# Kernel tuning notes

Hardware: AMD Instinct MI355X
Metric: run time of the kernel (lower is better)

The kernel has to match this reference:

```python
import jax, jax.numpy as jnp
import numpy as np

HEADS = 16
NEG = -1.0e9


def setup_inputs() -> dict:
    key = jax.random.key(0)
    ks = jax.random.split(key, 9)
    B, T, E = 2, 2048, 1024
    s = 1.0 / np.sqrt(E)
    return {
        "x": jax.random.normal(ks[0], (B, T, E), dtype=jnp.float32),
        "Wq": jax.random.normal(ks[1], (E, E), dtype=jnp.float32) * s,
        "bq": jax.random.normal(ks[2], (E,), dtype=jnp.float32) * 0.01,
        "Wk": jax.random.normal(ks[3], (E, E), dtype=jnp.float32) * s,
        "bk": jax.random.normal(ks[4], (E,), dtype=jnp.float32) * 0.01,
        "Wv": jax.random.normal(ks[5], (E, E), dtype=jnp.float32) * s,
        "bv": jax.random.normal(ks[6], (E,), dtype=jnp.float32) * 0.01,
        "Wo": jax.random.normal(ks[7], (E, E), dtype=jnp.float32) * s,
        "bo": jax.random.normal(ks[8], (E,), dtype=jnp.float32) * 0.01,
    }


def reference(x, Wq, bq, Wk, bk, Wv, bv, Wo, bo):
    B, T, E = x.shape
    H = HEADS
    D = E // H
    # In the original forward (idx_t=-2, context=None): context = x, so
    # values(x), keys(context), queries(context) all read x.
    v = (x @ Wv + bv).reshape(B, T, H, D)
    k = (x @ Wk + bk).reshape(B, T, H, D)
    q = (x @ Wq + bq).reshape(B, T, H, D)
    # causal mask: 1 above diagonal, 0 on/below; broadcast over (B, H)
    mask = 1.0 - jnp.tril(jnp.ones((T, T), dtype=x.dtype))  # [T, T]
    energy = jnp.einsum("bqhd,bkhd->bhqk", q, k)
    # Faithful to source: mask*(-1e9) added BEFORE the sqrt(embed_size) scaling
    energy = energy + mask[None, None] * jnp.asarray(NEG, dtype=x.dtype)
    attn = jax.nn.softmax(energy / jnp.sqrt(jnp.asarray(E, dtype=x.dtype)), axis=-1)
    out = jnp.einsum("bhqk,bkhd->bqhd", attn, v).reshape(B, T, E)
    return out @ Wo + bo
```

## Files before the change

### kernel.cpp

```cpp
#include <hip/hip_runtime.h>
#include <hip/hip_bf16.h>
#include <stdint.h>


typedef __attribute__((ext_vector_type(8))) short short8;
typedef __attribute__((ext_vector_type(4))) short short4v;
typedef __attribute__((ext_vector_type(4))) float f32x4;

#define MFMA16(a, b, c) __builtin_amdgcn_mfma_f32_16x16x32_bf16((a), (b), (c), 0, 0, 0)

static __device__ __forceinline__ unsigned short f2bf(float f) {
    union { float f; unsigned int u; } v; v.f = f;
    unsigned int r = v.u + 0x7fffu + ((v.u >> 16) & 1u);
    return (unsigned short)(r >> 16);
}
static __device__ __forceinline__ void gload16(const unsigned short* g,
                                               unsigned short* l) {
    __builtin_amdgcn_global_load_lds(
        (const __attribute__((address_space(1))) void*)g,
        (__attribute__((address_space(3))) void*)l, 16, 0, 0);
}

__global__ __launch_bounds__(256) void k_convert_x(const float* __restrict__ x,
                                                   unsigned short* __restrict__ xb) {
    int i = blockIdx.x * 256 + threadIdx.x;
    const float4* p = (const float4*)(x + (size_t)i * 8);
    float4 a = p[0], b = p[1];
    short8 o;
    o[0] = (short)f2bf(a.x); o[1] = (short)f2bf(a.y);
    o[2] = (short)f2bf(a.z); o[3] = (short)f2bf(a.w);
    o[4] = (short)f2bf(b.x); o[5] = (short)f2bf(b.y);
    o[6] = (short)f2bf(b.z); o[7] = (short)f2bf(b.w);
    ((short8*)xb)[i] = o;
}

__global__ __launch_bounds__(256) void k_transpose_w4(
        const float* __restrict__ W0, const float* __restrict__ W1,
        const float* __restrict__ W2, const float* __restrict__ W3,
        unsigned short* __restrict__ T0, unsigned short* __restrict__ T1,
        unsigned short* __restrict__ T2, unsigned short* __restrict__ T3) {
    const float* W = (blockIdx.z == 0) ? W0 : (blockIdx.z == 1) ? W1
                     : (blockIdx.z == 2) ? W2 : W3;
    unsigned short* Wt = (blockIdx.z == 0) ? T0 : (blockIdx.z == 1) ? T1
                         : (blockIdx.z == 2) ? T2 : T3;
    __shared__ float tw[64][68];
    const int k0 = blockIdx.x * 64, n0 = blockIdx.y * 64;
    const int tid = threadIdx.x;
#pragma unroll
    for (int r = 0; r < 4; ++r) {
        int i = tid + r * 256;
        int row = i >> 4, c4 = (i & 15) * 4;
        float4 v = *(const float4*)(W + (size_t)(k0 + row) * 1024 + n0 + c4);
        *(float4*)(&tw[row][c4]) = v;
    }
    __syncthreads();
#pragma unroll
    for (int r = 0; r < 2; ++r) {
        int i = tid + r * 256;
        int nrow = i >> 3, kc = (i & 7) * 8;
        short8 o;
#pragma unroll
        for (int j = 0; j < 8; ++j) o[j] = (short)f2bf(tw[kc + j][nrow]);
        *(short8*)(Wt + (size_t)(n0 + nrow) * 1024 + k0 + kc) = o;
    }
}

template <int MODE>
__global__ __launch_bounds__(256) void k_gemm2(const unsigned short* __restrict__ A,
                                               const unsigned short* __restrict__ Bt,
                                               const float* __restrict__ bq,
                                               const float* __restrict__ bk,
                                               const float* __restrict__ bv,
                                               unsigned short* __restrict__ Qb,
                                               unsigned short* __restrict__ Kb,
                                               unsigned short* __restrict__ Vt,
                                               float* __restrict__ Co) {
    __shared__ unsigned short As[128 * 32];
    __shared__ unsigned short Bs[128 * 32];
    const int tid = threadIdx.x;
    const int w = tid >> 6, lane = tid & 63;
    const int quad = lane >> 4, l16 = lane & 15;
    const int wm = w >> 1, wn = w & 1;
    const int m0 = blockIdx.x * 128, n0 = blockIdx.y * 128;
    const int lrow = lane >> 2, lch = (lane & 3) * 8;

    const unsigned short* ga = A + (size_t)(m0 + w * 32 + lrow) * 1024 + lch;
    const unsigned short* gb = Bt + (size_t)(n0 + w * 32 + lrow) * 1024 + lch;
    unsigned short* la0 = &As[(w * 32) * 32];
    unsigned short* la1 = &As[(w * 32 + 16) * 32];
    unsigned short* lb0 = &Bs[(w * 32) * 32];
    unsigned short* lb1 = &Bs[(w * 32 + 16) * 32];

    f32x4 acc[4][4];
#pragma unroll
    for (int mt = 0; mt < 4; ++mt)
#pragma unroll
        for (int nt = 0; nt < 4; ++nt) acc[mt][nt] = (f32x4){0.f, 0.f, 0.f, 0.f};

    for (int k0 = 0; k0 < 1024; k0 += 32) {
        __syncthreads();
        gload16(ga + k0, la0);
        gload16(ga + 16 * 1024 + k0, la1);
        gload16(gb + k0, lb0);
        gload16(gb + 16 * 1024 + k0, lb1);
        __syncthreads();
        short8 af[4], bf[4];
#pragma unroll
        for (int mt = 0; mt < 4; ++mt)
            af[mt] = *(const short8*)(&As[(wm * 64 + mt * 16 + l16) * 32 + quad * 8]);
#pragma unroll
        for (int nt = 0; nt < 4; ++nt)
            bf[nt] = *(const short8*)(&Bs[(wn * 64 + nt * 16 + l16) * 32 + quad * 8]);
#pragma unroll
        for (int mt = 0; mt < 4; ++mt)
#pragma unroll
            for (int nt = 0; nt < 4; ++nt)
                acc[mt][nt] = MFMA16(af[mt], bf[nt], acc[mt][nt]);
    }

    if (MODE == 1) {
#pragma unroll
        for (int nt = 0; nt < 4; ++nt) {
            int col = n0 + wn * 64 + nt * 16 + l16;
            float bb = bq[col];
#pragma unroll
            for (int mt = 0; mt < 4; ++mt) {
                int row = m0 + wm * 64 + mt * 16 + quad * 4;
#pragma unroll
                for (int r = 0; r < 4; ++r)
                    Co[(size_t)(row + r) * 1024 + col] = acc[mt][nt][r] + bb;
            }
        }
    } else if (n0 < 2048) {
        unsigned short* C = (n0 < 1024) ? Qb : Kb;
        const float* bias = (n0 < 1024) ? bq : bk;
        int cb = (n0 < 1024) ? n0 : (n0 - 1024);
#pragma unroll
        for (int nt = 0; nt < 4; ++nt) {
            int col = cb + wn * 64 + nt * 16 + l16;
            float bb = bias[col];
#pragma unroll
            for (int mt = 0; mt < 4; ++mt) {
                int row = m0 + wm * 64 + mt * 16 + quad * 4;
#pragma unroll
                for (int r = 0; r < 4; ++r)
                    C[(size_t)(row + r) * 1024 + col] = f2bf(acc[mt][nt][r] + bb);
            }
        }
    } else {
#pragma unroll
        for (int nt = 0; nt < 4; ++nt) {
            int vcol = (n0 - 2048) + wn * 64 + nt * 16 + l16;
            float bb = bv[vcol];
#pragma unroll
            for (int mt = 0; mt < 4; ++mt) {
                int row = m0 + wm * 64 + mt * 16 + quad * 4;
                int b = row >> 11, t = row & 2047;
                short4v o;
#pragma unroll
                for (int r = 0; r < 4; ++r) o[r] = (short)f2bf(acc[mt][nt][r] + bb);
                *(short4v*)(&Vt[((size_t)(b * 16 + (vcol >> 6)) * 64 + (vcol & 63))
                                    * 2048 + t]) = o;
            }
        }
    }
}

__global__ __launch_bounds__(256) void k_attn(const unsigned short* __restrict__ Qb,
                                              const unsigned short* __restrict__ Kb,
                                              const unsigned short* __restrict__ Vt,
                                              unsigned short* __restrict__ Ob) {
    __shared__ unsigned short Ks[2][64][72];
    __shared__ unsigned short Vs[2][64][72];
    __shared__ unsigned short Ps[4][16][72];
    const int tid = threadIdx.x;
    const int w = tid >> 6, lane = tid & 63;
    const int quad = lane >> 4, l16 = lane & 15;
    const int id = blockIdx.x;
    const int bh = (id & 7) + 8 * ((id >> 3) & 3);
    const int qb = 31 - (id >> 5);
    const int b = bh >> 4, h = bh & 15;
    const float scale = 0.03125f;
    const int qg = qb * 64 + w * 16 + l16;
    const f32x4 zero4 = {0.f, 0.f, 0.f, 0.f};

    const int srow = tid >> 3, sc8 = (tid & 7) * 8;
    const unsigned short* kg0 = Kb + (size_t)(b * 2048) * 1024 + h * 64 + sc8;
    const unsigned short* vg0 = Vt + (size_t)(bh * 64 + srow) * 2048 + sc8;

    short8 qf[2];
    {
        const unsigned short* qp =
            Qb + (size_t)(b * 2048 + qg) * 1024 + h * 64 + quad * 8;
        qf[0] = *(const short8*)(qp);
        qf[1] = *(const short8*)(qp + 32);
    }
    float m_ = -1e30f, l_ = 0.f;
    f32x4 o[4];
#pragma unroll
    for (int dt = 0; dt < 4; ++dt) o[dt] = zero4;

    short8 kr0, kr1, vr0, vr1;
    kr0 = *(const short8*)(kg0 + (size_t)(srow) * 1024);
    kr1 = *(const short8*)(kg0 + (size_t)(32 + srow) * 1024);
    vr0 = *(const short8*)(vg0);
    vr1 = *(const short8*)(vg0 + (size_t)32 * 2048);
    *(short8*)(&Ks[0][srow][sc8]) = kr0;
    *(short8*)(&Ks[0][32 + srow][sc8]) = kr1;
    *(short8*)(&Vs[0][srow][sc8]) = vr0;
    *(short8*)(&Vs[0][32 + srow][sc8]) = vr1;
    __syncthreads();

    for (int kt = 0; kt <= qb; ++kt) {
        const int cur = kt & 1;
        const bool more = kt < qb;
        if (more) {
            const unsigned short* kg = kg0 + (size_t)((kt + 1) * 64) * 1024;
            kr0 = *(const short8*)(kg + (size_t)(srow) * 1024);
            kr1 = *(const short8*)(kg + (size_t)(32 + srow) * 1024);
            vr0 = *(const short8*)(vg0 + (kt + 1) * 64);
            vr1 = *(const short8*)(vg0 + (size_t)32 * 2048 + (kt + 1) * 64);
        }

        f32x4 s[4];
#pragma unroll
        for (int kkt = 0; kkt < 4; ++kkt) {
            short8 kf0 = *(const short8*)(&Ks[cur][kkt * 16 + l16][quad * 8]);
            short8 kf1 = *(const short8*)(&Ks[cur][kkt * 16 + l16][32 + quad * 8]);
            s[kkt] = MFMA16(kf0, qf[0], zero4);
            s[kkt] = MFMA16(kf1, qf[1], s[kkt]);
        }

        float mx = -1e30f;
#pragma unroll
        for (int kkt = 0; kkt < 4; ++kkt) {
            int kg_ = kt * 64 + kkt * 16 + quad * 4;
#pragma unroll
            for (int r = 0; r < 4; ++r) {
                float v = s[kkt][r] * scale;
                v = (kt == qb && kg_ + r > qg) ? -1e30f : v;
                s[kkt][r] = v;
                mx = fmaxf(mx, v);
            }
        }
        mx = fmaxf(mx, __shfl_xor(mx, 16, 64));
        mx = fmaxf(mx, __shfl_xor(mx, 32, 64));
        float mn = fmaxf(m_, mx);
        float al = __expf(m_ - mn);
        m_ = mn;
        float sum = 0.f;
#pragma unroll
        for (int kkt = 0; kkt < 4; ++kkt)
#pragma unroll
            for (int r = 0; r < 4; ++r) {
                float p = __expf(s[kkt][r] - m_);
                s[kkt][r] = p;
                sum += p;
            }
        sum += __shfl_xor(sum, 16, 64);
        sum += __shfl_xor(sum, 32, 64);
        l_ = l_ * al + sum;
#pragma unroll
        for (int dt = 0; dt < 4; ++dt)
#pragma unroll
            for (int r = 0; r < 4; ++r) o[dt][r] *= al;

#pragma unroll
        for (int kkt = 0; kkt < 4; ++kkt) {
            short4v pk;
#pragma unroll
            for (int r = 0; r < 4; ++r) pk[r] = (short)f2bf(s[kkt][r]);
            *(short4v*)(&Ps[w][l16][kkt * 16 + quad * 4]) = pk;
        }
        __threadfence_block();

#pragma unroll
        for (int kks = 0; kks < 2; ++kks) {
            short8 pf = *(const short8*)(&Ps[w][l16][kks * 32 + quad * 8]);
#pragma unroll
            for (int dt = 0; dt < 4; ++dt) {
                short8 vf = *(const short8*)(
                    &Vs[cur][dt * 16 + l16][kks * 32 + quad * 8]);
                o[dt] = MFMA16(vf, pf, o[dt]);
            }
        }

        if (more) {
            const int nxt = cur ^ 1;
            *(short8*)(&Ks[nxt][srow][sc8]) = kr0;
            *(short8*)(&Ks[nxt][32 + srow][sc8]) = kr1;
            *(short8*)(&Vs[nxt][srow][sc8]) = vr0;
            *(short8*)(&Vs[nxt][32 + srow][sc8]) = vr1;
            __syncthreads();
        }
    }

    float inv = 1.0f / l_;
    unsigned short* op = Ob + (size_t)(b * 2048 + qg) * 1024 + h * 64 + quad * 4;
#pragma unroll
    for (int dt = 0; dt < 4; ++dt) {
        short4v ov;
#pragma unroll
        for (int r = 0; r < 4; ++r) ov[r] = (short)f2bf(o[dt][r] * inv);
        *(short4v*)(op + dt * 16) = ov;
    }
}

extern "C" void kernel_launch(void* const* d_in, const int* in_sizes, int n_in,
                              void* d_out, int out_size, void* d_ws, size_t ws_size,
                              hipStream_t stream) {
    const float* x  = (const float*)d_in[0];
    const float* Wq = (const float*)d_in[1];
    const float* bq = (const float*)d_in[2];
    const float* Wk = (const float*)d_in[3];
    const float* bk = (const float*)d_in[4];
    const float* Wv = (const float*)d_in[5];
    const float* bv = (const float*)d_in[6];
    const float* Wo = (const float*)d_in[7];
    const float* bo = (const float*)d_in[8];
    float* out = (float*)d_out;

    const size_t M4 = 4194304, M1 = 1048576;
    const size_t NEED = (M4 + M4 + 3 * M1 + M1) * 2;
    if (ws_size < NEED) return;
    unsigned short* ws = (unsigned short*)d_ws;
    unsigned short* xb  = ws;
    unsigned short* Ob  = ws;
    unsigned short* Vt  = ws + M4;
    unsigned short* WtQ = ws + 2 * M4;
    unsigned short* Wto = WtQ + 3 * M1;
    unsigned short* Qb  = (unsigned short*)d_out;
    unsigned short* Kb  = Qb + M4;

    k_convert_x<<<2048, 256, 0, stream>>>(x, xb);
    k_transpose_w4<<<dim3(16, 16, 4), 256, 0, stream>>>(
        Wq, Wk, Wv, Wo, WtQ, WtQ + M1, WtQ + 2 * M1, Wto);
    k_gemm2<0><<<dim3(32, 24), 256, 0, stream>>>(xb, WtQ, bq, bk, bv,
                                                 Qb, Kb, Vt, nullptr);
    k_attn<<<1024, 256, 0, stream>>>(Qb, Kb, Vt, Ob);
    k_gemm2<1><<<dim3(32, 8), 256, 0, stream>>>(Ob, Wto, bo, nullptr, nullptr,
                                                nullptr, nullptr, nullptr, out);
}
```

Measured before the change: 208.9 us.

## Double-buffer GEMM LDS tiles via registers; fold softmax scale into Q; skip redundant rescale

The GEMM main loop switches from direct global-to-LDS loads with two barriers per k-step to a register-staged double buffer. The next tile is prefetched into registers while MFMAs run on the current one, leaving one barrier per step. The 1/32 softmax scale is folded into the Q projection epilogue, and in attention the causal mask is applied only on the diagonal tile. The rescale of o and l is skipped when no lane's running max increased. This costs double the GEMM LDS footprint, more registers for the prefetch, and an extra bf16 rounding point for the scaled Q.

```diff
diff --git a/kernel.cpp b/kernel.cpp
--- a/kernel.cpp
+++ b/kernel.cpp
@@ -13,12 +13,6 @@
     union { float f; unsigned int u; } v; v.f = f;
     unsigned int r = v.u + 0x7fffu + ((v.u >> 16) & 1u);
     return (unsigned short)(r >> 16);
-}
-static __device__ __forceinline__ void gload16(const unsigned short* g,
-                                               unsigned short* l) {
-    __builtin_amdgcn_global_load_lds(
-        (const __attribute__((address_space(1))) void*)g,
-        (__attribute__((address_space(3))) void*)l, 16, 0, 0);
 }
 
 __global__ __launch_bounds__(256) void k_convert_x(const float* __restrict__ x,
@@ -75,8 +69,8 @@
                                                unsigned short* __restrict__ Kb,
                                                unsigned short* __restrict__ Vt,
                                                float* __restrict__ Co) {
-    __shared__ unsigned short As[128 * 32];
-    __shared__ unsigned short Bs[128 * 32];
+    __shared__ unsigned short As[2][128 * 32];
+    __shared__ unsigned short Bs[2][128 * 32];
     const int tid = threadIdx.x;
     const int w = tid >> 6, lane = tid & 63;
     const int quad = lane >> 4, l16 = lane & 15;
@@ -86,10 +80,7 @@
 
     const unsigned short* ga = A + (size_t)(m0 + w * 32 + lrow) * 1024 + lch;
     const unsigned short* gb = Bt + (size_t)(n0 + w * 32 + lrow) * 1024 + lch;
-    unsigned short* la0 = &As[(w * 32) * 32];
-    unsigned short* la1 = &As[(w * 32 + 16) * 32];
-    unsigned short* lb0 = &Bs[(w * 32) * 32];
-    unsigned short* lb1 = &Bs[(w * 32 + 16) * 32];
+    const int lofs = w * 1024 + lane * 8;
 
     f32x4 acc[4][4];
 #pragma unroll
@@ -97,25 +88,45 @@
 #pragma unroll
         for (int nt = 0; nt < 4; ++nt) acc[mt][nt] = (f32x4){0.f, 0.f, 0.f, 0.f};
 
+    short8 ar0 = *(const short8*)(ga);
+    short8 ar1 = *(const short8*)(ga + 16 * 1024);
+    short8 br0 = *(const short8*)(gb);
+    short8 br1 = *(const short8*)(gb + 16 * 1024);
+    *(short8*)(&As[0][lofs]) = ar0;
+    *(short8*)(&As[0][lofs + 512]) = ar1;
+    *(short8*)(&Bs[0][lofs]) = br0;
+    *(short8*)(&Bs[0][lofs + 512]) = br1;
+    __syncthreads();
+
     for (int k0 = 0; k0 < 1024; k0 += 32) {
-        __syncthreads();
-        gload16(ga + k0, la0);
-        gload16(ga + 16 * 1024 + k0, la1);
-        gload16(gb + k0, lb0);
-        gload16(gb + 16 * 1024 + k0, lb1);
-        __syncthreads();
+        const int cur = (k0 >> 5) & 1;
+        const bool more = (k0 + 32) < 1024;
+        if (more) {
+            ar0 = *(const short8*)(ga + k0 + 32);
+            ar1 = *(const short8*)(ga + 16 * 1024 + k0 + 32);
+            br0 = *(const short8*)(gb + k0 + 32);
+            br1 = *(const short8*)(gb + 16 * 1024 + k0 + 32);
+        }
         short8 af[4], bf[4];
 #pragma unroll
         for (int mt = 0; mt < 4; ++mt)
-            af[mt] = *(const short8*)(&As[(wm * 64 + mt * 16 + l16) * 32 + quad * 8]);
+            af[mt] = *(const short8*)(&As[cur][(wm * 64 + mt * 16 + l16) * 32 + quad * 8]);
 #pragma unroll
         for (int nt = 0; nt < 4; ++nt)
-            bf[nt] = *(const short8*)(&Bs[(wn * 64 + nt * 16 + l16) * 32 + quad * 8]);
+            bf[nt] = *(const short8*)(&Bs[cur][(wn * 64 + nt * 16 + l16) * 32 + quad * 8]);
 #pragma unroll
         for (int mt = 0; mt < 4; ++mt)
 #pragma unroll
             for (int nt = 0; nt < 4; ++nt)
                 acc[mt][nt] = MFMA16(af[mt], bf[nt], acc[mt][nt]);
+        if (more) {
+            const int nxt = cur ^ 1;
+            *(short8*)(&As[nxt][lofs]) = ar0;
+            *(short8*)(&As[nxt][lofs + 512]) = ar1;
+            *(short8*)(&Bs[nxt][lofs]) = br0;
+            *(short8*)(&Bs[nxt][lofs + 512]) = br1;
+            __syncthreads();
+        }
     }
 
     if (MODE == 1) {
@@ -134,6 +145,7 @@
     } else if (n0 < 2048) {
         unsigned short* C = (n0 < 1024) ? Qb : Kb;
         const float* bias = (n0 < 1024) ? bq : bk;
+        const float sc = (n0 < 1024) ? 0.03125f : 1.0f;
         int cb = (n0 < 1024) ? n0 : (n0 - 1024);
 #pragma unroll
         for (int nt = 0; nt < 4; ++nt) {
@@ -144,7 +156,7 @@
                 int row = m0 + wm * 64 + mt * 16 + quad * 4;
 #pragma unroll
                 for (int r = 0; r < 4; ++r)
-                    C[(size_t)(row + r) * 1024 + col] = f2bf(acc[mt][nt][r] + bb);
+                    C[(size_t)(row + r) * 1024 + col] = f2bf((acc[mt][nt][r] + bb) * sc);
             }
         }
     } else {
@@ -180,7 +192,6 @@
     const int bh = (id & 7) + 8 * ((id >> 3) & 3);
     const int qb = 31 - (id >> 5);
     const int b = bh >> 4, h = bh & 15;
-    const float scale = 0.03125f;
     const int qg = qb * 64 + w * 16 + l16;
     const f32x4 zero4 = {0.f, 0.f, 0.f, 0.f};
 
@@ -231,23 +242,24 @@
             s[kkt] = MFMA16(kf1, qf[1], s[kkt]);
         }
 
+        if (kt == qb) {
+#pragma unroll
+            for (int kkt = 0; kkt < 4; ++kkt) {
+                int kg_ = qb * 64 + kkt * 16 + quad * 4;
+#pragma unroll
+                for (int r = 0; r < 4; ++r)
+                    if (kg_ + r > qg) s[kkt][r] = -1e30f;
+            }
+        }
         float mx = -1e30f;
 #pragma unroll
-        for (int kkt = 0; kkt < 4; ++kkt) {
-            int kg_ = kt * 64 + kkt * 16 + quad * 4;
-#pragma unroll
-            for (int r = 0; r < 4; ++r) {
-                float v = s[kkt][r] * scale;
-                v = (kt == qb && kg_ + r > qg) ? -1e30f : v;
-                s[kkt][r] = v;
-                mx = fmaxf(mx, v);
-            }
-        }
+        for (int kkt = 0; kkt < 4; ++kkt)
+#pragma unroll
+            for (int r = 0; r < 4; ++r) mx = fmaxf(mx, s[kkt][r]);
         mx = fmaxf(mx, __shfl_xor(mx, 16, 64));
         mx = fmaxf(mx, __shfl_xor(mx, 32, 64));
-        float mn = fmaxf(m_, mx);
-        float al = __expf(m_ - mn);
-        m_ = mn;
+        const float mold = m_;
+        m_ = fmaxf(m_, mx);
         float sum = 0.f;
 #pragma unroll
         for (int kkt = 0; kkt < 4; ++kkt)
@@ -259,11 +271,16 @@
             }
         sum += __shfl_xor(sum, 16, 64);
         sum += __shfl_xor(sum, 32, 64);
-        l_ = l_ * al + sum;
-#pragma unroll
-        for (int dt = 0; dt < 4; ++dt)
-#pragma unroll
-            for (int r = 0; r < 4; ++r) o[dt][r] *= al;
+        if (__any(m_ > mold)) {
+            float al = __expf(mold - m_);
+            l_ = l_ * al + sum;
+#pragma unroll
+            for (int dt = 0; dt < 4; ++dt)
+#pragma unroll
+                for (int r = 0; r < 4; ++r) o[dt][r] *= al;
+        } else {
+            l_ += sum;
+        }
 
 #pragma unroll
         for (int kkt = 0; kkt < 4; ++kkt) {
```

Measured after the change: 204.4 us. 1.02x faster.
